# Kernel tuning notes

Hardware: AMD Instinct MI355X
Metric: run time of the kernel (lower is better)

## Reference

```python
import jax, jax.numpy as jnp
import numpy as np
import math

B, S, H, DM, DH = 4, 1024, 12, 768, 64


def setup_inputs() -> dict:
    key = jax.random.key(0)
    ks = jax.random.split(key, 5)
    std = 0.02
    return {
        "normalized_resid_pre": jax.random.normal(ks[0], (B, S, H, DM), dtype=jnp.float32),
        "W_Q": jax.random.normal(ks[1], (H, DM, DH), dtype=jnp.float32) * std,
        "b_Q": jnp.zeros((H, DH), dtype=jnp.float32),
        "W_K": jax.random.normal(ks[2], (H, DM, DH), dtype=jnp.float32) * std,
        "b_K": jnp.zeros((H, DH), dtype=jnp.float32),
        "W_V": jax.random.normal(ks[3], (H, DM, DH), dtype=jnp.float32) * std,
        "b_V": jnp.zeros((H, DH), dtype=jnp.float32),
        "W_O": jax.random.normal(ks[4], (H, DH, DM), dtype=jnp.float32) * std,
        "b_O": jnp.zeros((DM,), dtype=jnp.float32),
    }


def reference(normalized_resid_pre, W_Q, b_Q, W_K, b_K, W_V, b_V, W_O, b_O):
    x = normalized_resid_pre  # [B, S, H, DM]
    q = jnp.einsum("bshm,hmd->bshd", x, W_Q) + b_Q  # [B,S,H,DH]
    k = jnp.einsum("bshm,hmd->bshd", x, W_K) + b_K
    v = jnp.einsum("bshm,hmd->bshd", x, W_V) + b_V
    # positional_embedding_type == 'learned' -> no rotary applied
    scores = jnp.einsum("bqhd,bkhd->bhqk", q, k) / math.sqrt(DH)  # [B,H,S,S]
    causal = jnp.triu(jnp.ones((S, S), dtype=bool), k=1)  # True above diagonal
    scores = jnp.where(causal[None, None], -jnp.inf, scores)
    pattern = jax.nn.softmax(scores, axis=-1)
    pattern = jnp.where(jnp.isnan(pattern), 0.0, pattern)
    z = jnp.einsum("bhqk,bkhd->bqhd", pattern, v)  # [B,S,H,DH]
    # NOTE: per-head output (no sum over heads), bias split across heads
    attn_out = jnp.einsum("bqhd,hdm->bqhm", z, W_O) + b_O / H  # [B,S,H,DM]
    return attn_out
```

## Files before the change

### kernel.cpp

```cpp
#include <hip/hip_runtime.h>
#include <hip/hip_bf16.h>
#include <stdint.h>

constexpr int CB = 4, CS = 1024, CH = 12, CDM = 768, CDH = 64;
constexpr float QSCALE = 0.125f * 1.44269504088896340736f;
constexpr float SHIFT = 4.0f;

typedef __attribute__((ext_vector_type(8))) short bf16x8;
typedef __attribute__((ext_vector_type(4))) short bf16x4;
typedef __attribute__((ext_vector_type(4))) float f32x4;

__device__ inline short f2bf(float f) {
    union { __hip_bfloat16 h; short s; } u;
    u.h = __float2bfloat16(f);
    return u.s;
}
__device__ inline float exp2fast(float f) { return __builtin_amdgcn_exp2f(f); }

__global__ __launch_bounds__(256) void prep_kernel(
    const float* __restrict__ wq, const float* __restrict__ wk,
    const float* __restrict__ wv, const float* __restrict__ wo,
    short* __restrict__ wT, short* __restrict__ woT)
{
    const int blk = blockIdx.x;
    __shared__ short tile[64 * 65];
    const int tid = threadIdx.x;

    if (blk < 3 * CH * (CDM / 64)) {
        const int wsel = blk / (CH * (CDM / 64));
        const int rem = blk % (CH * (CDM / 64));
        const int h = rem / (CDM / 64);
        const int m0 = (rem % (CDM / 64)) * 64;
        const float* wp = (wsel == 0) ? wq : (wsel == 1) ? wk : wv;
        const float scale = (wsel == 0) ? QSCALE : 1.0f;
        #pragma unroll
        for (int it = 0; it < 16; ++it) {
            int i = it * 4 + (tid >> 6);
            int d = tid & 63;
            tile[i * 65 + d] = f2bf(wp[((size_t)h * CDM + m0 + i) * CDH + d] * scale);
        }
        __syncthreads();
        #pragma unroll
        for (int it = 0; it < 16; ++it) {
            int d = it * 4 + (tid >> 6);
            int m = tid & 63;
            wT[((size_t)(wsel * CH + h) * CDH + d) * CDM + m0 + m] = tile[m * 65 + d];
        }
    } else {
        const int r2 = blk - 3 * CH * (CDM / 64);
        const int h = r2 / (CDM / 64);
        const int m0 = (r2 % (CDM / 64)) * 64;
        #pragma unroll
        for (int it = 0; it < 16; ++it) {
            int d = it * 4 + (tid >> 6);
            int m = tid & 63;
            tile[m * 65 + d] = f2bf(wo[((size_t)h * CDH + d) * CDM + m0 + m]);
        }
        __syncthreads();
        #pragma unroll
        for (int it = 0; it < 16; ++it) {
            int m = it * 4 + (tid >> 6);
            int d = tid & 63;
            woT[((size_t)h * CDM + m0 + m) * CDH + d] = tile[m * 65 + d];
        }
    }
}

__global__ __launch_bounds__(256) void qkv_kernel(
    const float* __restrict__ x, const short* __restrict__ wT,
    const float* __restrict__ bq, const float* __restrict__ bk,
    const float* __restrict__ bv,
    short* __restrict__ q_ws, short* __restrict__ k_ws, short* __restrict__ vt_ws)
{
    const int h = blockIdx.y;
    const int row0 = blockIdx.x * 64;
    const int tid = threadIdx.x;
    const int w = tid >> 6;
    const int l = tid & 63;
    const int l15 = l & 15, lg = l >> 4;

    __shared__ short sbuf[2 * 12288];

    const f32x4 zero4 = {0.f, 0.f, 0.f, 0.f};
    f32x4 acc[12];
    #pragma unroll
    for (int i = 0; i < 12; ++i) acc[i] = zero4;

    const float* xrow = x + (size_t)(row0 + w * 16 + l15) * (CH * CDM) + h * CDM + lg * 8;

    const int r_lo = tid >> 3;
    const int s_phys = tid & 7;
    auto stage = [&](int bsel, int kk) {
        #pragma unroll
        for (int j = 0; j < 6; ++j) {
            int r = j * 32 + r_lo;
            int s_log = s_phys ^ (r & 7);
            const short* gp = wT + ((size_t)((r >> 6) * CH + h) * CDH + (r & 63)) * CDM
                              + kk + s_log * 8;
            short* lp = sbuf + bsel * 12288 + (j * 4096 + w * 1024) / 2;
            __builtin_amdgcn_global_load_lds(
                (const __attribute__((address_space(1))) uint32_t*)gp,
                (__attribute__((address_space(3))) uint32_t*)lp, 16, 0, 0);
        }
    };

    float4 xp0 = *(const float4*)(xrow);
    float4 xp1 = *(const float4*)(xrow + 4);
    float4 xp2 = *(const float4*)(xrow + 32);
    float4 xp3 = *(const float4*)(xrow + 36);
    stage(0, 0);
    asm volatile("s_waitcnt vmcnt(0)" ::: "memory");
    __syncthreads();

    for (int t = 0; t < 12; ++t) {
        const int kk = t * 64;
        bf16x8 A0, A1;
        A0[0] = f2bf(xp0.x); A0[1] = f2bf(xp0.y); A0[2] = f2bf(xp0.z); A0[3] = f2bf(xp0.w);
        A0[4] = f2bf(xp1.x); A0[5] = f2bf(xp1.y); A0[6] = f2bf(xp1.z); A0[7] = f2bf(xp1.w);
        A1[0] = f2bf(xp2.x); A1[1] = f2bf(xp2.y); A1[2] = f2bf(xp2.z); A1[3] = f2bf(xp2.w);
        A1[4] = f2bf(xp3.x); A1[5] = f2bf(xp3.y); A1[6] = f2bf(xp3.z); A1[7] = f2bf(xp3.w);

        if (t < 11) stage((t + 1) & 1, kk + 64);
        __builtin_amdgcn_sched_barrier(0);
        if (t < 11) {
            xp0 = *(const float4*)(xrow + kk + 64);
            xp1 = *(const float4*)(xrow + kk + 68);
            xp2 = *(const float4*)(xrow + kk + 96);
            xp3 = *(const float4*)(xrow + kk + 100);
        }

        const short* bb = sbuf + (t & 1) * 12288;
        #pragma unroll
        for (int ct = 0; ct < 12; ++ct) {
            int r = ct * 16 + l15;
            int sw = r & 7;
            bf16x8 b0 = *(const bf16x8*)(bb + r * 64 + ((lg ^ sw) << 3));
            bf16x8 b1 = *(const bf16x8*)(bb + r * 64 + (((4 | lg) ^ sw) << 3));
            acc[ct] = __builtin_amdgcn_mfma_f32_16x16x32_bf16(A0, b0, acc[ct], 0, 0, 0);
            acc[ct] = __builtin_amdgcn_mfma_f32_16x16x32_bf16(A1, b1, acc[ct], 0, 0, 0);
        }
        asm volatile("s_waitcnt vmcnt(4)" ::: "memory");
        __syncthreads();
    }

    const int b = row0 >> 10;
    const int sbase = row0 & (CS - 1);
    const size_t qkbase = (size_t)(b * CH + h) * CS;
    short* vt = sbuf;

    #pragma unroll
    for (int t = 0; t < 4; ++t) {
        int d = t * 16 + l15;
        float biasq = bq[h * CDH + d] * QSCALE;
        float biask = bk[h * CDH + d];
        float biasv = bv[h * CDH + d];
        #pragma unroll
        for (int r = 0; r < 4; ++r) {
            int s = sbase + w * 16 + lg * 4 + r;
            q_ws[(qkbase + s) * CDH + d] = f2bf(acc[t][r] + biasq);
            k_ws[(qkbase + s) * CDH + d] = f2bf(acc[4 + t][r] + biask);
            vt[d * 72 + (w * 16 + lg * 4 + r)] = f2bf(acc[8 + t][r] + biasv);
        }
    }
    __syncthreads();
    {
        int dd = tid >> 2;
        int s0 = (tid & 3) * 16;
        size_t vdst = ((size_t)(b * CH + h) * CDH + dd) * CS + sbase + s0;
        *(bf16x8*)(vt_ws + vdst)     = *(const bf16x8*)(&vt[dd * 72 + s0]);
        *(bf16x8*)(vt_ws + vdst + 8) = *(const bf16x8*)(&vt[dd * 72 + s0 + 8]);
    }
}

__global__ __launch_bounds__(256) void attn_out_kernel(
    const short* __restrict__ q_ws, const short* __restrict__ k_ws,
    const short* __restrict__ vt_ws, const short* __restrict__ woT,
    const float* __restrict__ bo, float* __restrict__ out)
{
    const int f = blockIdx.x;
    const int xcd = f & 7;
    const int s = f >> 3;
    const int r_rank = (s < 32) ? s : (s < 64 ? 95 - s : s);
    const int c = 15 - (r_rank / 6);
    const int bh = xcd + 8 * (r_rank % 6);
    const int b = bh / CH, h = bh % CH;
    const int tid = threadIdx.x;
    const int wv = tid >> 6, l = tid & 63;
    const int l15 = l & 15, lg = l >> 4;
    const int q0w = c * 64 + wv * 16;

    __shared__ short kvbuf[2][8192];
    __shared__ short pls_all[4][16 * 72];

    short* pls = &pls_all[wv][0];
    const short* kg = k_ws + (size_t)bh * CS * CDH;
    const short* vg = vt_ws + (size_t)bh * CDH * CS;

    const short* qp = q_ws + ((size_t)bh * CS + q0w + l15) * CDH + lg * 8;
    bf16x8 aq0 = *(const bf16x8*)(qp);
    bf16x8 aq1 = *(const bf16x8*)(qp + 32);

    const f32x4 zero4 = {0.f, 0.f, 0.f, 0.f};
    f32x4 acc_o[4];
    #pragma unroll
    for (int j = 0; j < 4; ++j) acc_o[j] = zero4;
    float l_r = 0.f;

    auto stage = [&](int bsel, int t) {
        #pragma unroll
        for (int j = 0; j < 2; ++j) {
            int slot = j * 256 + tid;
            int row = slot >> 3;
            int sl = (slot & 7) ^ (row & 7);
            const short* gk = kg + (size_t)(t * 64 + row) * CDH + sl * 8;
            const short* gv = vg + (size_t)row * CS + t * 64 + sl * 8;
            short* lk = &kvbuf[bsel][(j * 256 + wv * 64) * 8];
            short* lv = &kvbuf[bsel][4096 + (j * 256 + wv * 64) * 8];
            __builtin_amdgcn_global_load_lds(
                (const __attribute__((address_space(1))) uint32_t*)gk,
                (__attribute__((address_space(3))) uint32_t*)lk, 16, 0, 0);
            __builtin_amdgcn_global_load_lds(
                (const __attribute__((address_space(1))) uint32_t*)gv,
                (__attribute__((address_space(3))) uint32_t*)lv, 16, 0, 0);
        }
    };

    const int T = c + 1;

    stage(0, 0);
    asm volatile("s_waitcnt vmcnt(0)" ::: "memory");
    __syncthreads();

    for (int t = 0; t < T; ++t) {
        if (t + 1 < T) stage((t + 1) & 1, t + 1);

        const short* kb = kvbuf[t & 1];
        const short* vb = kvbuf[t & 1] + 4096;
        bf16x8 kf[4][2];
        #pragma unroll
        for (int j = 0; j < 4; ++j) {
            int row = j * 16 + l15, sw = row & 7;
            kf[j][0] = *(const bf16x8*)(kb + row * 64 + ((lg ^ sw) << 3));
            kf[j][1] = *(const bf16x8*)(kb + row * 64 + (((4 | lg) ^ sw) << 3));
        }
        bf16x4 vf16[4][4];
        #pragma unroll
        for (int j = 0; j < 4; ++j)
            #pragma unroll
            for (int ct = 0; ct < 4; ++ct) {
                int row = ct * 16 + l15;
                int slot = (2 * j + (lg >> 1)) ^ (row & 7);
                vf16[j][ct] = *(const bf16x4*)(vb + row * 64 + slot * 8 + 4 * (lg & 1));
            }

        f32x4 s4[4];
        __builtin_amdgcn_s_setprio(1);
        #pragma unroll
        for (int j = 0; j < 4; ++j) {
            s4[j] = __builtin_amdgcn_mfma_f32_16x16x32_bf16(kf[j][0], aq0, zero4, 0, 0, 0);
            s4[j] = __builtin_amdgcn_mfma_f32_16x16x32_bf16(kf[j][1], aq1, s4[j], 0, 0, 0);
        }
        __builtin_amdgcn_s_setprio(0);
        if (t == T - 1) {
            #pragma unroll
            for (int j = 0; j < 4; ++j)
                #pragma unroll
                for (int r = 0; r < 4; ++r)
                    if (t * 64 + j * 16 + lg * 4 + r > q0w + l15)
                        s4[j][r] = -1e30f;
        }
        bf16x4 pj[4];
        #pragma unroll
        for (int j = 0; j < 4; ++j) {
            float p0 = exp2fast(s4[j][0] - SHIFT);
            float p1 = exp2fast(s4[j][1] - SHIFT);
            float p2 = exp2fast(s4[j][2] - SHIFT);
            float p3 = exp2fast(s4[j][3] - SHIFT);
            l_r += (p0 + p1) + (p2 + p3);
            pj[j][0] = f2bf(p0); pj[j][1] = f2bf(p1);
            pj[j][2] = f2bf(p2); pj[j][3] = f2bf(p3);
        }
        __builtin_amdgcn_s_setprio(1);
        #pragma unroll
        for (int j = 0; j < 4; ++j)
            #pragma unroll
            for (int ct = 0; ct < 4; ++ct)
                acc_o[ct] = __builtin_amdgcn_mfma_f32_16x16x16bf16_1k(
                    pj[j], vf16[j][ct], acc_o[ct], 0, 0, 0);
        __builtin_amdgcn_s_setprio(0);

        asm volatile("s_waitcnt vmcnt(0)" ::: "memory");
        __syncthreads();
    }

    float rs = l_r;
    rs += __shfl_xor(rs, 16);
    rs += __shfl_xor(rs, 32);
    float invq[4];
    #pragma unroll
    for (int r = 0; r < 4; ++r) invq[r] = 1.0f / __shfl(rs, lg * 4 + r);

    #pragma unroll
    for (int r = 0; r < 4; ++r) {
        short* zr = pls + (lg * 4 + r) * 72 + l15;
        zr[0]  = f2bf(acc_o[0][r] * invq[r]);
        zr[16] = f2bf(acc_o[1][r] * invq[r]);
        zr[32] = f2bf(acc_o[2][r] * invq[r]);
        zr[48] = f2bf(acc_o[3][r] * invq[r]);
    }
    asm volatile("s_waitcnt lgkmcnt(0)" ::: "memory");
    bf16x8 a0 = *(const bf16x8*)(&pls[l15 * 72 + lg * 8]);
    bf16x8 a1 = *(const bf16x8*)(&pls[l15 * 72 + 32 + lg * 8]);

    const short* wo_h = woT + (size_t)h * CDM * CDH;
    float* obase = out + ((size_t)(b * CS + q0w) * CH + h) * CDM;
    float* fst = (float*)(&kvbuf[0][0]) + (size_t)wv * (16 * 68);

    for (int ch = 0; ch < 12; ++ch) {
        asm volatile("s_waitcnt lgkmcnt(0)" ::: "memory");
        #pragma unroll
        for (int ct2 = 0; ct2 < 4; ++ct2) {
            int ct = ch * 4 + ct2;
            const short* wb = wo_h + (size_t)(ct * 16 + l15) * CDH + lg * 8;
            bf16x8 b0 = *(const bf16x8*)(wb);
            bf16x8 b1 = *(const bf16x8*)(wb + 32);
            f32x4 acc = __builtin_amdgcn_mfma_f32_16x16x32_bf16(a0, b0, zero4, 0, 0, 0);
            acc = __builtin_amdgcn_mfma_f32_16x16x32_bf16(a1, b1, acc, 0, 0, 0);
            float bias = bo[ct * 16 + l15] * (1.0f / CH);
            #pragma unroll
            for (int r = 0; r < 4; ++r)
                fst[(lg * 4 + r) * 68 + ct2 * 16 + l15] = acc[r] + bias;
        }
        asm volatile("s_waitcnt lgkmcnt(0)" ::: "memory");
        #pragma unroll
        for (int it = 0; it < 4; ++it) {
            int idx = it * 64 + l;
            int row = idx >> 4;
            int c4 = idx & 15;
            float4 v = *(const float4*)(fst + row * 68 + c4 * 4);
            *(float4*)(obase + (size_t)row * (CH * CDM) + ch * 64 + c4 * 4) = v;
        }
    }
}

extern "C" void kernel_launch(void* const* d_in, const int* in_sizes, int n_in,
                              void* d_out, int out_size, void* d_ws, size_t ws_size,
                              hipStream_t stream) {
    const float* x  = (const float*)d_in[0];
    const float* wq = (const float*)d_in[1];
    const float* bq = (const float*)d_in[2];
    const float* wk = (const float*)d_in[3];
    const float* bk = (const float*)d_in[4];
    const float* wv = (const float*)d_in[5];
    const float* bv = (const float*)d_in[6];
    const float* wo = (const float*)d_in[7];
    const float* bo = (const float*)d_in[8];
    float* out = (float*)d_out;

    const size_t tsz = (size_t)CB * CH * CS * CDH;
    short* q_ws  = (short*)d_ws;
    short* k_ws  = q_ws + tsz;
    short* vt_ws = k_ws + tsz;
    short* z_ws  = vt_ws + tsz;
    short* wT  = z_ws;
    short* woT = z_ws + (size_t)3 * CH * CDH * CDM;

    prep_kernel<<<dim3(4 * CH * (CDM / 64)), 256, 0, stream>>>(
        wq, wk, wv, wo, wT, woT);
    qkv_kernel<<<dim3(CB * CS / 64, CH), 256, 0, stream>>>(
        x, wT, bq, bk, bv, q_ws, k_ws, vt_ws);
    attn_out_kernel<<<dim3(16 * CB * CH), 256, 0, stream>>>(
        q_ws, k_ws, vt_ws, woT, bo, out);
}
```

Before: 114.7 us.

## Triple-buffer K/V tiles with one barrier per step in attention kernel

Changes the K/V LDS staging from double to triple buffering and prefetches two tiles ahead. The loop now does a partial vmcnt wait and one barrier per iteration instead of a full drain plus barrier after each tile, and the masked final tile is peeled out. The separate per-wave P buffer is folded into the shared kvbuf region for the epilogue, and the kernel asks for 3 blocks per SM via launch bounds. This adds LDS pressure, 48KB per block, and relies on the vmcnt counts being correct.

```diff
diff --git a/kernel.cpp b/kernel.cpp
--- a/kernel.cpp
+++ b/kernel.cpp
@@ -172,7 +172,7 @@
     }
 }
 
-__global__ __launch_bounds__(256) void attn_out_kernel(
+__global__ __launch_bounds__(256, 3) void attn_out_kernel(
     const short* __restrict__ q_ws, const short* __restrict__ k_ws,
     const short* __restrict__ vt_ws, const short* __restrict__ woT,
     const float* __restrict__ bo, float* __restrict__ out)
@@ -189,10 +189,9 @@
     const int l15 = l & 15, lg = l >> 4;
     const int q0w = c * 64 + wv * 16;
 
-    __shared__ short kvbuf[2][8192];
-    __shared__ short pls_all[4][16 * 72];
-
-    short* pls = &pls_all[wv][0];
+    __shared__ short kvbuf[3][8192];
+    short* lds_base = &kvbuf[0][0];
+
     const short* kg = k_ws + (size_t)bh * CS * CDH;
     const short* vg = vt_ws + (size_t)bh * CDH * CS;
 
@@ -225,17 +224,9 @@
         }
     };
 
-    const int T = c + 1;
-
-    stage(0, 0);
-    asm volatile("s_waitcnt vmcnt(0)" ::: "memory");
-    __syncthreads();
-
-    for (int t = 0; t < T; ++t) {
-        if (t + 1 < T) stage((t + 1) & 1, t + 1);
-
-        const short* kb = kvbuf[t & 1];
-        const short* vb = kvbuf[t & 1] + 4096;
+    auto body = [&](int t, bool masked) {
+        const short* kb = kvbuf[t % 3];
+        const short* vb = kvbuf[t % 3] + 4096;
         bf16x8 kf[4][2];
         #pragma unroll
         for (int j = 0; j < 4; ++j) {
@@ -261,7 +252,7 @@
             s4[j] = __builtin_amdgcn_mfma_f32_16x16x32_bf16(kf[j][1], aq1, s4[j], 0, 0, 0);
         }
         __builtin_amdgcn_s_setprio(0);
-        if (t == T - 1) {
+        if (masked) {
             #pragma unroll
             for (int j = 0; j < 4; ++j)
                 #pragma unroll
@@ -288,10 +279,35 @@
                 acc_o[ct] = __builtin_amdgcn_mfma_f32_16x16x16bf16_1k(
                     pj[j], vf16[j][ct], acc_o[ct], 0, 0, 0);
         __builtin_amdgcn_s_setprio(0);
-
-        asm volatile("s_waitcnt vmcnt(0)" ::: "memory");
-        __syncthreads();
-    }
+    };
+
+    const int T = c + 1;
+
+    stage(0, 0);
+    if (T > 1) stage(1, 1);
+
+    for (int t = 0; t + 2 < T; ++t) {
+        asm volatile("s_waitcnt vmcnt(4)" ::: "memory");
+        __builtin_amdgcn_s_barrier();
+        asm volatile("" ::: "memory");
+        stage((t + 2) % 3, t + 2);
+        body(t, false);
+    }
+    if (T >= 2) {
+        asm volatile("s_waitcnt vmcnt(4)" ::: "memory");
+        __builtin_amdgcn_s_barrier();
+        asm volatile("" ::: "memory");
+        body(T - 2, false);
+    }
+    asm volatile("s_waitcnt vmcnt(0)" ::: "memory");
+    __builtin_amdgcn_s_barrier();
+    asm volatile("" ::: "memory");
+    body(T - 1, true);
+    __builtin_amdgcn_s_barrier();
+    asm volatile("" ::: "memory");
+
+    float* fst = (float*)lds_base + (size_t)wv * (16 * 68);
+    short* plsE = lds_base + 8704 + wv * 1152;
 
     float rs = l_r;
     rs += __shfl_xor(rs, 16);
@@ -302,19 +318,18 @@
 
     #pragma unroll
     for (int r = 0; r < 4; ++r) {
-        short* zr = pls + (lg * 4 + r) * 72 + l15;
+        short* zr = plsE + (lg * 4 + r) * 72 + l15;
         zr[0]  = f2bf(acc_o[0][r] * invq[r]);
         zr[16] = f2bf(acc_o[1][r] * invq[r]);
         zr[32] = f2bf(acc_o[2][r] * invq[r]);
         zr[48] = f2bf(acc_o[3][r] * invq[r]);
     }
     asm volatile("s_waitcnt lgkmcnt(0)" ::: "memory");
-    bf16x8 a0 = *(const bf16x8*)(&pls[l15 * 72 + lg * 8]);
-    bf16x8 a1 = *(const bf16x8*)(&pls[l15 * 72 + 32 + lg * 8]);
+    bf16x8 a0 = *(const bf16x8*)(&plsE[l15 * 72 + lg * 8]);
+    bf16x8 a1 = *(const bf16x8*)(&plsE[l15 * 72 + 32 + lg * 8]);
 
     const short* wo_h = woT + (size_t)h * CDM * CDH;
     float* obase = out + ((size_t)(b * CS + q0w) * CH + h) * CDM;
-    float* fst = (float*)(&kvbuf[0][0]) + (size_t)wv * (16 * 68);
 
     for (int ch = 0; ch < 12; ++ch) {
         asm volatile("s_waitcnt lgkmcnt(0)" ::: "memory");
```

New measurement: 114.0 us. Within noise of the previous version (-0.5%).
